# Kernel tuning notes

Measured on AMD Instinct MI355X. Metric: run time of the kernel, lower is better.

## Reference

```python
import jax, jax.numpy as jnp
import numpy as np

N = 8192
D_IN = 512
D_HID = 256
D_OUT = 128
NEG_SLOPE = 0.25
MASK_VAL = -1.0e12
EDGE_PROB = 0.004  # avg degree ~33


def _leaky(x):
    return jax.nn.leaky_relu(x, NEG_SLOPE)


def setup_inputs() -> dict:
    key = jax.random.key(0)
    ks = jax.random.split(key, 9)
    x = jax.random.normal(ks[0], (N, D_IN), jnp.float32)
    # sparse-ish normalized adjacency, stored dense (torch uses sparse mm / to_dense)
    vals = jax.random.uniform(ks[1], (N, N), jnp.float32)
    mask = jax.random.uniform(ks[2], (N, N)) < EDGE_PROB
    adj = jnp.where(mask, vals, 0.0).astype(jnp.float32)
    W1 = jax.random.normal(ks[3], (D_IN, D_HID), jnp.float32) * (2.0 / (D_IN + D_HID)) ** 0.5
    b1 = jnp.zeros((D_HID,), jnp.float32)
    W2 = jax.random.normal(ks[4], (D_HID, D_HID), jnp.float32) * (1.0 / D_HID) ** 0.5
    b2 = jnp.zeros((D_HID,), jnp.float32)
    Wg = jax.random.normal(ks[5], (D_HID, D_OUT), jnp.float32) * (2.0 / (D_HID + D_OUT)) ** 0.5
    a = jax.random.normal(ks[6], (2 * D_OUT, 1), jnp.float32) * 0.1
    return dict(x=x, adj=adj, W1=W1, b1=b1, W2=W2, b2=b2, Wg=Wg, a=a)


def reference(x, adj, W1, b1, W2, b2, Wg, a):
    # GCN layer 1: adj @ (x @ W1) + b1, leaky_relu (dropout p=0 / eval -> identity)
    x1 = _leaky(adj @ (x @ W1) + b1)
    # GCN layer 2
    x2 = _leaky(adj @ (x1 @ W2) + b2)
    # GAT layer: h = x2 @ Wg; e[i,j] = leaky_relu([h_i || h_j] @ a)
    # identical to leaky_relu((h@a1)_i + (h@a2)_j) without the O(N^2*2F) concat
    h = x2 @ Wg                              # [N, D_OUT]
    a1 = a[:D_OUT, 0]
    a2 = a[D_OUT:, 0]
    e = _leaky((h @ a1)[:, None] + (h @ a2)[None, :])  # [N, N]
    att = jnp.where(adj > 0, e, MASK_VAL)
    att = jax.nn.softmax(att, axis=1)
    h_prime = att @ h                        # [N, D_OUT] (concat=False -> no elu)
    out = _leaky(h_prime)
    mu = out[:, : D_OUT // 2]
    logvar = out[:, D_OUT // 2 :]
    return mu, logvar
```

## Files before the change

kernel.cpp:

```cpp
#include <hip/hip_runtime.h>

typedef unsigned short u16;
typedef u16 u16x4 __attribute__((ext_vector_type(4)));
typedef __bf16 bf16x8 __attribute__((ext_vector_type(8)));
typedef float f32x4 __attribute__((ext_vector_type(4)));

#define NROW 8192
#define CAP 128
#define D_IN 512
#define D_HID 256
#define D_OUT 128

__device__ __forceinline__ float leaky_f(float x) { return x > 0.f ? x : 0.25f * x; }

__device__ __forceinline__ u16 f2bf_rne(float f) {
  unsigned u = __float_as_uint(f);
  u += 0x7fffu + ((u >> 16) & 1u);
  return (u16)(u >> 16);
}
__device__ __forceinline__ float bf2f(u16 v) { return __uint_as_float(((unsigned)v) << 16); }
__device__ __forceinline__ void split_bf16(float f, u16& hi, u16& lo) {
  hi = f2bf_rne(f);
  float fh = __uint_as_float(((unsigned)hi) << 16);
  lo = f2bf_rne(f - fh);
}

__global__ __launch_bounds__(256) void k_packw(
    const float* __restrict__ W1, u16* __restrict__ B1,
    const float* __restrict__ W2, u16* __restrict__ B2,
    const float* __restrict__ Wg, u16* __restrict__ B3) {
  const float* W; u16* Bt; int K, Nc, id;
  int pb = blockIdx.x;
  if (pb < 512)      { W = W1; Bt = B1; K = D_IN;  Nc = D_HID; id = pb * 256 + threadIdx.x; }
  else if (pb < 768) { W = W2; Bt = B2; K = D_HID; Nc = D_HID; id = (pb - 512) * 256 + threadIdx.x; }
  else               { W = Wg; Bt = B3; K = D_HID; Nc = D_OUT; id = (pb - 768) * 256 + threadIdx.x; }
  int n = id % Nc, k = id / Nc;
  float f = W[id];
  u16 hi, lo; split_bf16(f, hi, lo);
  size_t ro = (size_t)n * 2 * K;
  Bt[ro + k] = hi; Bt[ro + K + k] = lo;
}

__global__ __launch_bounds__(256) void k_csr_gemm1(const float* __restrict__ adj,
    int* __restrict__ cnt, int* __restrict__ cols, float* __restrict__ vals,
    const float* __restrict__ X, const u16* __restrict__ Bt, float* __restrict__ C) {
  __shared__ u16 Ah[64 * 40], Al[64 * 40];
  __shared__ u16 Bh[64 * 40], Bl[64 * 40];
  __shared__ int csrc;
  int b = blockIdx.x;
  int tid = threadIdx.x;
  if (b < 512) {
    const int N = D_HID, K = D_IN;
    int bm = (b >> 2) * 64, bn = (b & 3) * 64;
    int wave = tid >> 6, lane = tid & 63, l15 = lane & 15, quad = lane >> 4;
    f32x4 acc[4] = {};
    int ar = tid >> 2, aj = (tid & 3) << 3;
    const float* Xrow = X + (size_t)(bm + ar) * K + aj;
    const u16* Brow = Bt + (size_t)(bn + ar) * (2 * K) + aj;
    for (int k0 = 0; k0 < K; k0 += 32) {
      alignas(16) u16 hh[8], ll[8];
      float xv[8];
      *(float4*)(xv)     = *(const float4*)(Xrow + k0);
      *(float4*)(xv + 4) = *(const float4*)(Xrow + k0 + 4);
#pragma unroll
      for (int e = 0; e < 8; ++e) split_bf16(xv[e], hh[e], ll[e]);
      *(uint4*)(&Ah[ar * 40 + aj]) = *(const uint4*)hh;
      *(uint4*)(&Al[ar * 40 + aj]) = *(const uint4*)ll;
      *(uint4*)(&Bh[ar * 40 + aj]) = *(const uint4*)(Brow + k0);
      *(uint4*)(&Bl[ar * 40 + aj]) = *(const uint4*)(Brow + K + k0);
      __syncthreads();
      bf16x8 afh = *(const bf16x8*)(&Ah[(wave * 16 + l15) * 40 + quad * 8]);
      bf16x8 afl = *(const bf16x8*)(&Al[(wave * 16 + l15) * 40 + quad * 8]);
#pragma unroll
      for (int c = 0; c < 4; ++c) {
        bf16x8 bfh = *(const bf16x8*)(&Bh[(c * 16 + l15) * 40 + quad * 8]);
        bf16x8 bfl = *(const bf16x8*)(&Bl[(c * 16 + l15) * 40 + quad * 8]);
        acc[c] = __builtin_amdgcn_mfma_f32_16x16x32_bf16(afh, bfh, acc[c], 0, 0, 0);
        acc[c] = __builtin_amdgcn_mfma_f32_16x16x32_bf16(afh, bfl, acc[c], 0, 0, 0);
        acc[c] = __builtin_amdgcn_mfma_f32_16x16x32_bf16(afl, bfh, acc[c], 0, 0, 0);
      }
      __syncthreads();
    }
#pragma unroll
    for (int c = 0; c < 4; ++c)
#pragma unroll
      for (int rg = 0; rg < 4; ++rg) {
        int rowi = bm + wave * 16 + quad * 4 + rg;
        int coli = bn + c * 16 + l15;
        C[(size_t)rowi * N + coli] = acc[c][rg];
      }
    return;
  }
  int i = b - 512;
  if (tid == 0) csrc = 0;
  __syncthreads();
  const float4* row = (const float4*)(adj + (size_t)i * NROW);
  for (int j4 = tid; j4 < NROW / 4; j4 += 256) {
    float4 v = row[j4];
    int base = j4 * 4;
    if (v.x > 0.f) { int s = atomicAdd(&csrc, 1); if (s < CAP) { cols[i*CAP+s] = base;   vals[i*CAP+s] = v.x; } }
    if (v.y > 0.f) { int s = atomicAdd(&csrc, 1); if (s < CAP) { cols[i*CAP+s] = base+1; vals[i*CAP+s] = v.y; } }
    if (v.z > 0.f) { int s = atomicAdd(&csrc, 1); if (s < CAP) { cols[i*CAP+s] = base+2; vals[i*CAP+s] = v.z; } }
    if (v.w > 0.f) { int s = atomicAdd(&csrc, 1); if (s < CAP) { cols[i*CAP+s] = base+3; vals[i*CAP+s] = v.w; } }
  }
  __syncthreads();
  if (tid == 0) cnt[i] = (csrc < CAP) ? csrc : CAP;
}

__global__ __launch_bounds__(256) void k_gemm(const u16* __restrict__ A, const u16* __restrict__ Bt,
    float* __restrict__ C, int N, int K) {
  __shared__ u16 Ah[64 * 40], Al[64 * 40];
  __shared__ u16 Bh[64 * 40], Bl[64 * 40];
  int tid = threadIdx.x;
  int bm = blockIdx.y * 64, bn = blockIdx.x * 64;
  int wave = tid >> 6, lane = tid & 63, l15 = lane & 15, quad = lane >> 4;
  f32x4 acc[4] = {};
  int ar = tid >> 2, aj = (tid & 3) << 3;
  const u16* Arow = A + (size_t)(bm + ar) * (2 * K) + aj;
  const u16* Brow = Bt + (size_t)(bn + ar) * (2 * K) + aj;
  for (int k0 = 0; k0 < K; k0 += 32) {
    *(uint4*)(&Ah[ar * 40 + aj]) = *(const uint4*)(Arow + k0);
    *(uint4*)(&Al[ar * 40 + aj]) = *(const uint4*)(Arow + K + k0);
    *(uint4*)(&Bh[ar * 40 + aj]) = *(const uint4*)(Brow + k0);
    *(uint4*)(&Bl[ar * 40 + aj]) = *(const uint4*)(Brow + K + k0);
    __syncthreads();
    bf16x8 afh = *(const bf16x8*)(&Ah[(wave * 16 + l15) * 40 + quad * 8]);
    bf16x8 afl = *(const bf16x8*)(&Al[(wave * 16 + l15) * 40 + quad * 8]);
#pragma unroll
    for (int c = 0; c < 4; ++c) {
      bf16x8 bfh = *(const bf16x8*)(&Bh[(c * 16 + l15) * 40 + quad * 8]);
      bf16x8 bfl = *(const bf16x8*)(&Bl[(c * 16 + l15) * 40 + quad * 8]);
      acc[c] = __builtin_amdgcn_mfma_f32_16x16x32_bf16(afh, bfh, acc[c], 0, 0, 0);
      acc[c] = __builtin_amdgcn_mfma_f32_16x16x32_bf16(afh, bfl, acc[c], 0, 0, 0);
      acc[c] = __builtin_amdgcn_mfma_f32_16x16x32_bf16(afl, bfh, acc[c], 0, 0, 0);
    }
    __syncthreads();
  }
#pragma unroll
  for (int c = 0; c < 4; ++c)
#pragma unroll
    for (int rg = 0; rg < 4; ++rg) {
      int rowi = bm + wave * 16 + quad * 4 + rg;
      int coli = bn + c * 16 + l15;
      C[(size_t)rowi * N + coli] = acc[c][rg];
    }
}

__global__ __launch_bounds__(256) void k_gemm3(const u16* __restrict__ A, const u16* __restrict__ Bt,
    u16* __restrict__ Hb, int K,
    const float* __restrict__ aptr, float* __restrict__ s1, float* __restrict__ s2) {
  __shared__ u16 Ah[32 * 40], Al[32 * 40];
  __shared__ u16 Bh[128 * 40], Bl[128 * 40];
  __shared__ float sp1[2][32], sp2[2][32];
  int tid = threadIdx.x;
  int bm = blockIdx.y * 32;
  int wave = tid >> 6, lane = tid & 63, l15 = lane & 15, quad = lane >> 4;
  int rhalf = wave >> 1, chalf = wave & 1;
  f32x4 acc[4] = {};
  int t7 = tid & 127;
  int ar = t7 >> 2, aj = (t7 & 3) << 3;
  int br = tid >> 1, bj = (tid & 1) << 4;
  const u16* Arow = A + (size_t)(bm + ar) * (2 * K) + aj + (tid < 128 ? 0 : K);
  u16* Adst = (tid < 128 ? Ah : Al) + ar * 40 + aj;
  const u16* Brow = Bt + (size_t)br * (2 * K) + bj;
  for (int k0 = 0; k0 < K; k0 += 32) {
    *(uint4*)Adst = *(const uint4*)(Arow + k0);
#pragma unroll
    for (int jj = 0; jj < 2; ++jj) {
      *(uint4*)(&Bh[br * 40 + bj + jj * 8]) = *(const uint4*)(Brow + k0 + jj * 8);
      *(uint4*)(&Bl[br * 40 + bj + jj * 8]) = *(const uint4*)(Brow + K + k0 + jj * 8);
    }
    __syncthreads();
    bf16x8 afh = *(const bf16x8*)(&Ah[(rhalf * 16 + l15) * 40 + quad * 8]);
    bf16x8 afl = *(const bf16x8*)(&Al[(rhalf * 16 + l15) * 40 + quad * 8]);
#pragma unroll
    for (int c = 0; c < 4; ++c) {
      bf16x8 bfh = *(const bf16x8*)(&Bh[(chalf * 64 + c * 16 + l15) * 40 + quad * 8]);
      bf16x8 bfl = *(const bf16x8*)(&Bl[(chalf * 64 + c * 16 + l15) * 40 + quad * 8]);
      acc[c] = __builtin_amdgcn_mfma_f32_16x16x32_bf16(afh, bfh, acc[c], 0, 0, 0);
      acc[c] = __builtin_amdgcn_mfma_f32_16x16x32_bf16(afh, bfl, acc[c], 0, 0, 0);
      acc[c] = __builtin_amdgcn_mfma_f32_16x16x32_bf16(afl, bfh, acc[c], 0, 0, 0);
    }
    __syncthreads();
  }
#pragma unroll
  for (int c = 0; c < 4; ++c)
#pragma unroll
    for (int rg = 0; rg < 4; ++rg) {
      int rowi = bm + rhalf * 16 + quad * 4 + rg;
      int coli = chalf * 64 + c * 16 + l15;
      Hb[(size_t)rowi * 128 + coli] = f2bf_rne(acc[c][rg]);
    }
  float a1v[4], a2v[4];
#pragma unroll
  for (int c = 0; c < 4; ++c) {
    a1v[c] = aptr[chalf * 64 + c * 16 + l15];
    a2v[c] = aptr[128 + chalf * 64 + c * 16 + l15];
  }
#pragma unroll
  for (int rg = 0; rg < 4; ++rg) {
    float p1 = 0.f, p2 = 0.f;
#pragma unroll
    for (int c = 0; c < 4; ++c) { p1 = fmaf(acc[c][rg], a1v[c], p1); p2 = fmaf(acc[c][rg], a2v[c], p2); }
#pragma unroll
    for (int m = 1; m < 16; m <<= 1) { p1 += __shfl_xor(p1, m); p2 += __shfl_xor(p2, m); }
    if (l15 == 0) {
      int rloc = rhalf * 16 + quad * 4 + rg;
      sp1[chalf][rloc] = p1; sp2[chalf][rloc] = p2;
    }
  }
  __syncthreads();
  if (tid < 32) {
    s1[bm + tid] = sp1[0][tid] + sp1[1][tid];
    s2[bm + tid] = sp2[0][tid] + sp2[1][tid];
  }
}

__global__ __launch_bounds__(256) void k_spmm_pack(const float* __restrict__ Hin,
    const float* __restrict__ bias, const int* __restrict__ cnt,
    const int* __restrict__ cols, const float* __restrict__ vals, u16* __restrict__ Ap) {
  int i = blockIdx.x, t = threadIdx.x;
  int t64 = t & 63, g = t >> 6;
  __shared__ int sc[CAP];
  __shared__ float sv[CAP];
  __shared__ float4 sacc[4][64];
  int n = cnt[i];
  if (t < n) { sc[t] = cols[i * CAP + t]; sv[t] = vals[i * CAP + t]; }
  __syncthreads();
  float4 acc = {0.f, 0.f, 0.f, 0.f};
  const float4* H4 = (const float4*)Hin;
  for (int k = g; k < n; k += 4) {
    float w = sv[k];
    float4 v = H4[(size_t)sc[k] * 64 + t64];
    acc.x = fmaf(w, v.x, acc.x); acc.y = fmaf(w, v.y, acc.y);
    acc.z = fmaf(w, v.z, acc.z); acc.w = fmaf(w, v.w, acc.w);
  }
  sacc[g][t64] = acc;
  __syncthreads();
  if (t < 64) {
    float4 a0 = sacc[0][t], a1 = sacc[1][t], a2 = sacc[2][t], a3 = sacc[3][t];
    float4 bv = ((const float4*)bias)[t];
    float r[4] = { leaky_f(a0.x + a1.x + a2.x + a3.x + bv.x),
                   leaky_f(a0.y + a1.y + a2.y + a3.y + bv.y),
                   leaky_f(a0.z + a1.z + a2.z + a3.z + bv.z),
                   leaky_f(a0.w + a1.w + a2.w + a3.w + bv.w) };
    u16x4 hi4, lo4;
#pragma unroll
    for (int e = 0; e < 4; ++e) { u16 hh, ll; split_bf16(r[e], hh, ll); hi4[e] = hh; lo4[e] = ll; }
    size_t ro = (size_t)i * 512;
    *(u16x4*)(Ap + ro + 4 * t) = hi4;
    *(u16x4*)(Ap + ro + 256 + 4 * t) = lo4;
  }
}

__global__ __launch_bounds__(128) void k_attn(const u16* __restrict__ Hb,
    const float* __restrict__ s1, const float* __restrict__ s2,
    const int* __restrict__ cnt, const int* __restrict__ cols, float* __restrict__ out) {
  int i = blockIdx.x, t = threadIdx.x;
  int t32 = t & 31, g = t >> 5;
  __shared__ int sc[CAP];
  __shared__ float sw[CAP];
  __shared__ float sred[2];
  __shared__ float4 sacc[4][32];
  int n = cnt[i];
  float s1i = s1[i];
  if (t < n) { int c = cols[i * CAP + t]; sc[t] = c; sw[t] = leaky_f(s1i + s2[c]); }
  __syncthreads();
  if (t < 64) {
    float m = -1e30f;
    if (t < n) m = sw[t];
    if (t + 64 < n) m = fmaxf(m, sw[t + 64]);
    for (int o = 32; o > 0; o >>= 1) m = fmaxf(m, __shfl_down(m, o));
    if (t == 0) sred[0] = m;
  }
  __syncthreads();
  float mx = sred[0];
  if (t < n) sw[t] = expf(sw[t] - mx);
  __syncthreads();
  if (t < 64) {
    float s = 0.f;
    if (t < n) s = sw[t];
    if (t + 64 < n) s += sw[t + 64];
    for (int o = 32; o > 0; o >>= 1) s += __shfl_down(s, o);
    if (t == 0) sred[1] = s;
  }
  __syncthreads();
  float inv = (n > 0) ? 1.0f / sred[1] : 0.f;
  float4 acc = {0.f, 0.f, 0.f, 0.f};
  for (int k = g; k < n; k += 4) {
    float w = sw[k];
    u16x4 v = *(const u16x4*)(Hb + (size_t)sc[k] * 128 + 4 * t32);
    acc.x = fmaf(w, bf2f(v[0]), acc.x); acc.y = fmaf(w, bf2f(v[1]), acc.y);
    acc.z = fmaf(w, bf2f(v[2]), acc.z); acc.w = fmaf(w, bf2f(v[3]), acc.w);
  }
  sacc[g][t32] = acc;
  __syncthreads();
  if (t < 32) {
    float4 a0 = sacc[0][t], a1 = sacc[1][t], a2 = sacc[2][t], a3 = sacc[3][t];
    float4 r;
    r.x = leaky_f((a0.x + a1.x + a2.x + a3.x) * inv);
    r.y = leaky_f((a0.y + a1.y + a2.y + a3.y) * inv);
    r.z = leaky_f((a0.z + a1.z + a2.z + a3.z) * inv);
    r.w = leaky_f((a0.w + a1.w + a2.w + a3.w) * inv);
    float4* o4 = (float4*)out;
    if (t < 16) o4[(size_t)i * 16 + t] = r;
    else        o4[(size_t)NROW * 16 + (size_t)i * 16 + (t - 16)] = r;
  }
}

extern "C" void kernel_launch(void* const* d_in, const int* in_sizes, int n_in,
                              void* d_out, int out_size, void* d_ws, size_t ws_size,
                              hipStream_t stream) {
  const float* x   = (const float*)d_in[0];
  const float* adj = (const float*)d_in[1];
  const float* W1  = (const float*)d_in[2];
  const float* b1  = (const float*)d_in[3];
  const float* W2  = (const float*)d_in[4];
  const float* b2  = (const float*)d_in[5];
  const float* Wg  = (const float*)d_in[6];
  const float* a   = (const float*)d_in[7];
  float* out = (float*)d_out;

  char* ws = (char*)d_ws;
  int*   row_cnt  = (int*)  (ws + 0);
  int*   row_cols = (int*)  (ws + 32768);
  float* row_vals = (float*)(ws + 4227072);
  u16*   B1t      = (u16*)  (ws + 8421376);
  u16*   B2t      = (u16*)  (ws + 8945664);
  u16*   B3t      = (u16*)  (ws + 9207808);
  float* s1       = (float*)(ws + 9338880);
  float* s2       = (float*)(ws + 9371648);
  u16*   hbf      = (u16*)  (ws + 9404416);
  float* H0T2     = (float*)(ws + 13598720);
  u16*   Apack    = (u16*)  (ws + 21987328);

  k_packw<<<896, 256, 0, stream>>>(W1, B1t, W2, B2t, Wg, B3t);
  k_csr_gemm1<<<512 + NROW, 256, 0, stream>>>(adj, row_cnt, row_cols, row_vals, x, B1t, H0T2);
  k_spmm_pack<<<NROW, 256, 0, stream>>>(H0T2, b1, row_cnt, row_cols, row_vals, Apack);
  k_gemm<<<dim3(4, 128), 256, 0, stream>>>(Apack, B2t, H0T2, D_HID, D_HID);
  k_spmm_pack<<<NROW, 256, 0, stream>>>(H0T2, b2, row_cnt, row_cols, row_vals, Apack);
  k_gemm3<<<dim3(1, 256), 256, 0, stream>>>(Apack, B3t, hbf, D_HID, a, s1, s2);
  k_attn<<<NROW, 128, 0, stream>>>(hbf, s1, s2, row_cnt, row_cols, out);
}
```

Baseline: 471.9 us.

## Fuse sparse aggregation with following dense GEMM in layers two and three

Each sparse adjacency aggregation (bias, leaky ReLU, bf16 hi/lo split) now runs inside the same kernel as the following dense GEMM. Sixteen aggregated rows are kept in shared memory and fed directly to MFMA, which removes the packed activation round-trip through global memory and two kernel launches. In exchange only 512 blocks are launched, and each wave gathers its rows serially without the previous 4-way split over neighbours. Every block also reloads the full weight matrix, so occupancy and gather latency may suffer.

```diff
diff --git a/kernel.cpp b/kernel.cpp
--- a/kernel.cpp
+++ b/kernel.cpp
@@ -107,32 +107,60 @@
   if (tid == 0) cnt[i] = (csrc < CAP) ? csrc : CAP;
 }
 
-__global__ __launch_bounds__(256) void k_gemm(const u16* __restrict__ A, const u16* __restrict__ Bt,
-    float* __restrict__ C, int N, int K) {
-  __shared__ u16 Ah[64 * 40], Al[64 * 40];
-  __shared__ u16 Bh[64 * 40], Bl[64 * 40];
-  int tid = threadIdx.x;
-  int bm = blockIdx.y * 64, bn = blockIdx.x * 64;
-  int wave = tid >> 6, lane = tid & 63, l15 = lane & 15, quad = lane >> 4;
-  f32x4 acc[4] = {};
-  int ar = tid >> 2, aj = (tid & 3) << 3;
-  const u16* Arow = A + (size_t)(bm + ar) * (2 * K) + aj;
-  const u16* Brow = Bt + (size_t)(bn + ar) * (2 * K) + aj;
-  for (int k0 = 0; k0 < K; k0 += 32) {
-    *(uint4*)(&Ah[ar * 40 + aj]) = *(const uint4*)(Arow + k0);
-    *(uint4*)(&Al[ar * 40 + aj]) = *(const uint4*)(Arow + K + k0);
-    *(uint4*)(&Bh[ar * 40 + aj]) = *(const uint4*)(Brow + k0);
-    *(uint4*)(&Bl[ar * 40 + aj]) = *(const uint4*)(Brow + K + k0);
-    __syncthreads();
-    bf16x8 afh = *(const bf16x8*)(&Ah[(wave * 16 + l15) * 40 + quad * 8]);
-    bf16x8 afl = *(const bf16x8*)(&Al[(wave * 16 + l15) * 40 + quad * 8]);
+__global__ __launch_bounds__(256) void k_spmm_gemm2(const float* __restrict__ Hin,
+    const float* __restrict__ bias, const int* __restrict__ cnt,
+    const int* __restrict__ cols, const float* __restrict__ vals,
+    const u16* __restrict__ Bt, float* __restrict__ T2) {
+  __shared__ u16 Ahh[16 * 264], All[16 * 264];
+  __shared__ u16 Bh[256 * 40], Bl[256 * 40];
+  __shared__ int scw[4][CAP];
+  __shared__ float svw[4][CAP];
+  int tid = threadIdx.x, wave = tid >> 6, lane = tid & 63;
+  int base = blockIdx.x * 16;
+  const float4* H4 = (const float4*)Hin;
+  float4 bv = ((const float4*)bias)[lane];
+  for (int rr = 0; rr < 4; ++rr) {
+    int row = base + wave * 4 + rr;
+    int n = cnt[row];
+    if (lane < n)      { scw[wave][lane]      = cols[row*CAP+lane];      svw[wave][lane]      = vals[row*CAP+lane]; }
+    if (lane + 64 < n) { scw[wave][lane+64]   = cols[row*CAP+lane+64];   svw[wave][lane+64]   = vals[row*CAP+lane+64]; }
+    __syncthreads();
+    float4 acc = {0.f, 0.f, 0.f, 0.f};
+    for (int k = 0; k < n; ++k) {
+      float w = svw[wave][k];
+      float4 v = H4[(size_t)scw[wave][k] * 64 + lane];
+      acc.x = fmaf(w, v.x, acc.x); acc.y = fmaf(w, v.y, acc.y);
+      acc.z = fmaf(w, v.z, acc.z); acc.w = fmaf(w, v.w, acc.w);
+    }
+    float r[4] = { leaky_f(acc.x + bv.x), leaky_f(acc.y + bv.y),
+                   leaky_f(acc.z + bv.z), leaky_f(acc.w + bv.w) };
+    u16x4 hi4, lo4;
+#pragma unroll
+    for (int e = 0; e < 4; ++e) { u16 hh, ll; split_bf16(r[e], hh, ll); hi4[e] = hh; lo4[e] = ll; }
+    int ra = wave * 4 + rr;
+    *(u16x4*)(&Ahh[ra * 264 + lane * 4]) = hi4;
+    *(u16x4*)(&All[ra * 264 + lane * 4]) = lo4;
+    __syncthreads();
+  }
+  int l15 = lane & 15, quad = lane >> 4;
+  f32x4 acc2[4] = {};
+  for (int k0 = 0; k0 < 256; k0 += 32) {
+    const u16* Brow = Bt + (size_t)tid * 512 + k0;
+#pragma unroll
+    for (int j = 0; j < 4; ++j) {
+      *(uint4*)(&Bh[tid * 40 + j * 8]) = *(const uint4*)(Brow + j * 8);
+      *(uint4*)(&Bl[tid * 40 + j * 8]) = *(const uint4*)(Brow + 256 + j * 8);
+    }
+    __syncthreads();
+    bf16x8 afh = *(const bf16x8*)(&Ahh[l15 * 264 + k0 + quad * 8]);
+    bf16x8 afl = *(const bf16x8*)(&All[l15 * 264 + k0 + quad * 8]);
 #pragma unroll
     for (int c = 0; c < 4; ++c) {
-      bf16x8 bfh = *(const bf16x8*)(&Bh[(c * 16 + l15) * 40 + quad * 8]);
-      bf16x8 bfl = *(const bf16x8*)(&Bl[(c * 16 + l15) * 40 + quad * 8]);
-      acc[c] = __builtin_amdgcn_mfma_f32_16x16x32_bf16(afh, bfh, acc[c], 0, 0, 0);
-      acc[c] = __builtin_amdgcn_mfma_f32_16x16x32_bf16(afh, bfl, acc[c], 0, 0, 0);
-      acc[c] = __builtin_amdgcn_mfma_f32_16x16x32_bf16(afl, bfh, acc[c], 0, 0, 0);
+      bf16x8 bfh = *(const bf16x8*)(&Bh[(wave * 64 + c * 16 + l15) * 40 + quad * 8]);
+      bf16x8 bfl = *(const bf16x8*)(&Bl[(wave * 64 + c * 16 + l15) * 40 + quad * 8]);
+      acc2[c] = __builtin_amdgcn_mfma_f32_16x16x32_bf16(afh, bfh, acc2[c], 0, 0, 0);
+      acc2[c] = __builtin_amdgcn_mfma_f32_16x16x32_bf16(afh, bfl, acc2[c], 0, 0, 0);
+      acc2[c] = __builtin_amdgcn_mfma_f32_16x16x32_bf16(afl, bfh, acc2[c], 0, 0, 0);
     }
     __syncthreads();
   }
@@ -140,116 +168,97 @@
   for (int c = 0; c < 4; ++c)
 #pragma unroll
     for (int rg = 0; rg < 4; ++rg) {
-      int rowi = bm + wave * 16 + quad * 4 + rg;
-      int coli = bn + c * 16 + l15;
-      C[(size_t)rowi * N + coli] = acc[c][rg];
-    }
-}
-
-__global__ __launch_bounds__(256) void k_gemm3(const u16* __restrict__ A, const u16* __restrict__ Bt,
-    u16* __restrict__ Hb, int K,
+      int rowi = base + quad * 4 + rg;
+      int coli = wave * 64 + c * 16 + l15;
+      T2[(size_t)rowi * 256 + coli] = acc2[c][rg];
+    }
+}
+
+__global__ __launch_bounds__(256) void k_spmm_gemm3(const float* __restrict__ Hin,
+    const float* __restrict__ bias, const int* __restrict__ cnt,
+    const int* __restrict__ cols, const float* __restrict__ vals,
+    const u16* __restrict__ Bt, u16* __restrict__ Hb,
     const float* __restrict__ aptr, float* __restrict__ s1, float* __restrict__ s2) {
-  __shared__ u16 Ah[32 * 40], Al[32 * 40];
+  __shared__ u16 Ahh[16 * 264], All[16 * 264];
   __shared__ u16 Bh[128 * 40], Bl[128 * 40];
-  __shared__ float sp1[2][32], sp2[2][32];
-  int tid = threadIdx.x;
-  int bm = blockIdx.y * 32;
-  int wave = tid >> 6, lane = tid & 63, l15 = lane & 15, quad = lane >> 4;
-  int rhalf = wave >> 1, chalf = wave & 1;
-  f32x4 acc[4] = {};
-  int t7 = tid & 127;
-  int ar = t7 >> 2, aj = (t7 & 3) << 3;
-  int br = tid >> 1, bj = (tid & 1) << 4;
-  const u16* Arow = A + (size_t)(bm + ar) * (2 * K) + aj + (tid < 128 ? 0 : K);
-  u16* Adst = (tid < 128 ? Ah : Al) + ar * 40 + aj;
-  const u16* Brow = Bt + (size_t)br * (2 * K) + bj;
-  for (int k0 = 0; k0 < K; k0 += 32) {
-    *(uint4*)Adst = *(const uint4*)(Arow + k0);
-#pragma unroll
-    for (int jj = 0; jj < 2; ++jj) {
-      *(uint4*)(&Bh[br * 40 + bj + jj * 8]) = *(const uint4*)(Brow + k0 + jj * 8);
-      *(uint4*)(&Bl[br * 40 + bj + jj * 8]) = *(const uint4*)(Brow + K + k0 + jj * 8);
-    }
-    __syncthreads();
-    bf16x8 afh = *(const bf16x8*)(&Ah[(rhalf * 16 + l15) * 40 + quad * 8]);
-    bf16x8 afl = *(const bf16x8*)(&Al[(rhalf * 16 + l15) * 40 + quad * 8]);
-#pragma unroll
-    for (int c = 0; c < 4; ++c) {
-      bf16x8 bfh = *(const bf16x8*)(&Bh[(chalf * 64 + c * 16 + l15) * 40 + quad * 8]);
-      bf16x8 bfl = *(const bf16x8*)(&Bl[(chalf * 64 + c * 16 + l15) * 40 + quad * 8]);
-      acc[c] = __builtin_amdgcn_mfma_f32_16x16x32_bf16(afh, bfh, acc[c], 0, 0, 0);
-      acc[c] = __builtin_amdgcn_mfma_f32_16x16x32_bf16(afh, bfl, acc[c], 0, 0, 0);
-      acc[c] = __builtin_amdgcn_mfma_f32_16x16x32_bf16(afl, bfh, acc[c], 0, 0, 0);
-    }
-    __syncthreads();
-  }
-#pragma unroll
-  for (int c = 0; c < 4; ++c)
+  __shared__ int scw[4][CAP];
+  __shared__ float svw[4][CAP];
+  __shared__ float sp1[4][16], sp2[4][16];
+  int tid = threadIdx.x, wave = tid >> 6, lane = tid & 63;
+  int base = blockIdx.x * 16;
+  const float4* H4 = (const float4*)Hin;
+  float4 bv = ((const float4*)bias)[lane];
+  for (int rr = 0; rr < 4; ++rr) {
+    int row = base + wave * 4 + rr;
+    int n = cnt[row];
+    if (lane < n)      { scw[wave][lane]      = cols[row*CAP+lane];      svw[wave][lane]      = vals[row*CAP+lane]; }
+    if (lane + 64 < n) { scw[wave][lane+64]   = cols[row*CAP+lane+64];   svw[wave][lane+64]   = vals[row*CAP+lane+64]; }
+    __syncthreads();
+    float4 acc = {0.f, 0.f, 0.f, 0.f};
+    for (int k = 0; k < n; ++k) {
+      float w = svw[wave][k];
+      float4 v = H4[(size_t)scw[wave][k] * 64 + lane];
+      acc.x = fmaf(w, v.x, acc.x); acc.y = fmaf(w, v.y, acc.y);
+      acc.z = fmaf(w, v.z, acc.z); acc.w = fmaf(w, v.w, acc.w);
+    }
+    float r[4] = { leaky_f(acc.x + bv.x), leaky_f(acc.y + bv.y),
+                   leaky_f(acc.z + bv.z), leaky_f(acc.w + bv.w) };
+    u16x4 hi4, lo4;
+#pragma unroll
+    for (int e = 0; e < 4; ++e) { u16 hh, ll; split_bf16(r[e], hh, ll); hi4[e] = hh; lo4[e] = ll; }
+    int ra = wave * 4 + rr;
+    *(u16x4*)(&Ahh[ra * 264 + lane * 4]) = hi4;
+    *(u16x4*)(&All[ra * 264 + lane * 4]) = lo4;
+    __syncthreads();
+  }
+  int l15 = lane & 15, quad = lane >> 4;
+  f32x4 acc2[2] = {};
+  for (int k0 = 0; k0 < 256; k0 += 32) {
+    int n = tid & 127, half = tid >> 7;
+    const u16* Brow = Bt + (size_t)n * 512 + half * 256 + k0;
+    u16* dst = (half ? Bl : Bh) + n * 40;
+#pragma unroll
+    for (int j = 0; j < 4; ++j)
+      *(uint4*)(dst + j * 8) = *(const uint4*)(Brow + j * 8);
+    __syncthreads();
+    bf16x8 afh = *(const bf16x8*)(&Ahh[l15 * 264 + k0 + quad * 8]);
+    bf16x8 afl = *(const bf16x8*)(&All[l15 * 264 + k0 + quad * 8]);
+#pragma unroll
+    for (int c = 0; c < 2; ++c) {
+      bf16x8 bfh = *(const bf16x8*)(&Bh[((wave * 2 + c) * 16 + l15) * 40 + quad * 8]);
+      bf16x8 bfl = *(const bf16x8*)(&Bl[((wave * 2 + c) * 16 + l15) * 40 + quad * 8]);
+      acc2[c] = __builtin_amdgcn_mfma_f32_16x16x32_bf16(afh, bfh, acc2[c], 0, 0, 0);
+      acc2[c] = __builtin_amdgcn_mfma_f32_16x16x32_bf16(afh, bfl, acc2[c], 0, 0, 0);
+      acc2[c] = __builtin_amdgcn_mfma_f32_16x16x32_bf16(afl, bfh, acc2[c], 0, 0, 0);
+    }
+    __syncthreads();
+  }
+#pragma unroll
+  for (int c = 0; c < 2; ++c)
 #pragma unroll
     for (int rg = 0; rg < 4; ++rg) {
-      int rowi = bm + rhalf * 16 + quad * 4 + rg;
-      int coli = chalf * 64 + c * 16 + l15;
-      Hb[(size_t)rowi * 128 + coli] = f2bf_rne(acc[c][rg]);
-    }
-  float a1v[4], a2v[4];
-#pragma unroll
-  for (int c = 0; c < 4; ++c) {
-    a1v[c] = aptr[chalf * 64 + c * 16 + l15];
-    a2v[c] = aptr[128 + chalf * 64 + c * 16 + l15];
+      int rowi = base + quad * 4 + rg;
+      int coli = wave * 32 + c * 16 + l15;
+      Hb[(size_t)rowi * 128 + coli] = f2bf_rne(acc2[c][rg]);
+    }
+  float a1v[2], a2v[2];
+#pragma unroll
+  for (int c = 0; c < 2; ++c) {
+    a1v[c] = aptr[wave * 32 + c * 16 + l15];
+    a2v[c] = aptr[128 + wave * 32 + c * 16 + l15];
   }
 #pragma unroll
   for (int rg = 0; rg < 4; ++rg) {
-    float p1 = 0.f, p2 = 0.f;
-#pragma unroll
-    for (int c = 0; c < 4; ++c) { p1 = fmaf(acc[c][rg], a1v[c], p1); p2 = fmaf(acc[c][rg], a2v[c], p2); }
+    float p1 = fmaf(acc2[0][rg], a1v[0], acc2[1][rg] * a1v[1]);
+    float p2 = fmaf(acc2[0][rg], a2v[0], acc2[1][rg] * a2v[1]);
 #pragma unroll
     for (int m = 1; m < 16; m <<= 1) { p1 += __shfl_xor(p1, m); p2 += __shfl_xor(p2, m); }
-    if (l15 == 0) {
-      int rloc = rhalf * 16 + quad * 4 + rg;
-      sp1[chalf][rloc] = p1; sp2[chalf][rloc] = p2;
-    }
-  }
-  __syncthreads();
-  if (tid < 32) {
-    s1[bm + tid] = sp1[0][tid] + sp1[1][tid];
-    s2[bm + tid] = sp2[0][tid] + sp2[1][tid];
-  }
-}
-
-__global__ __launch_bounds__(256) void k_spmm_pack(const float* __restrict__ Hin,
-    const float* __restrict__ bias, const int* __restrict__ cnt,
-    const int* __restrict__ cols, const float* __restrict__ vals, u16* __restrict__ Ap) {
-  int i = blockIdx.x, t = threadIdx.x;
-  int t64 = t & 63, g = t >> 6;
-  __shared__ int sc[CAP];
-  __shared__ float sv[CAP];
-  __shared__ float4 sacc[4][64];
-  int n = cnt[i];
-  if (t < n) { sc[t] = cols[i * CAP + t]; sv[t] = vals[i * CAP + t]; }
-  __syncthreads();
-  float4 acc = {0.f, 0.f, 0.f, 0.f};
-  const float4* H4 = (const float4*)Hin;
-  for (int k = g; k < n; k += 4) {
-    float w = sv[k];
-    float4 v = H4[(size_t)sc[k] * 64 + t64];
-    acc.x = fmaf(w, v.x, acc.x); acc.y = fmaf(w, v.y, acc.y);
-    acc.z = fmaf(w, v.z, acc.z); acc.w = fmaf(w, v.w, acc.w);
-  }
-  sacc[g][t64] = acc;
-  __syncthreads();
-  if (t < 64) {
-    float4 a0 = sacc[0][t], a1 = sacc[1][t], a2 = sacc[2][t], a3 = sacc[3][t];
-    float4 bv = ((const float4*)bias)[t];
-    float r[4] = { leaky_f(a0.x + a1.x + a2.x + a3.x + bv.x),
-                   leaky_f(a0.y + a1.y + a2.y + a3.y + bv.y),
-                   leaky_f(a0.z + a1.z + a2.z + a3.z + bv.z),
-                   leaky_f(a0.w + a1.w + a2.w + a3.w + bv.w) };
-    u16x4 hi4, lo4;
-#pragma unroll
-    for (int e = 0; e < 4; ++e) { u16 hh, ll; split_bf16(r[e], hh, ll); hi4[e] = hh; lo4[e] = ll; }
-    size_t ro = (size_t)i * 512;
-    *(u16x4*)(Ap + ro + 4 * t) = hi4;
-    *(u16x4*)(Ap + ro + 256 + 4 * t) = lo4;
+    if (l15 == 0) { sp1[wave][quad * 4 + rg] = p1; sp2[wave][quad * 4 + rg] = p2; }
+  }
+  __syncthreads();
+  if (tid < 16) {
+    s1[base + tid] = sp1[0][tid] + sp1[1][tid] + sp1[2][tid] + sp1[3][tid];
+    s2[base + tid] = sp2[0][tid] + sp2[1][tid] + sp2[2][tid] + sp2[3][tid];
   }
 }
 
@@ -331,14 +340,12 @@
   float* s1       = (float*)(ws + 9338880);
   float* s2       = (float*)(ws + 9371648);
   u16*   hbf      = (u16*)  (ws + 9404416);
-  float* H0T2     = (float*)(ws + 13598720);
-  u16*   Apack    = (u16*)  (ws + 21987328);
+  float* H0       = (float*)(ws + 13598720);
+  float* T2       = (float*)(ws + 21987328);
 
   k_packw<<<896, 256, 0, stream>>>(W1, B1t, W2, B2t, Wg, B3t);
-  k_csr_gemm1<<<512 + NROW, 256, 0, stream>>>(adj, row_cnt, row_cols, row_vals, x, B1t, H0T2);
-  k_spmm_pack<<<NROW, 256, 0, stream>>>(H0T2, b1, row_cnt, row_cols, row_vals, Apack);
-  k_gemm<<<dim3(4, 128), 256, 0, stream>>>(Apack, B2t, H0T2, D_HID, D_HID);
-  k_spmm_pack<<<NROW, 256, 0, stream>>>(H0T2, b2, row_cnt, row_cols, row_vals, Apack);
-  k_gemm3<<<dim3(1, 256), 256, 0, stream>>>(Apack, B3t, hbf, D_HID, a, s1, s2);
+  k_csr_gemm1<<<512 + NROW, 256, 0, stream>>>(adj, row_cnt, row_cols, row_vals, x, B1t, H0);
+  k_spmm_gemm2<<<512, 256, 0, stream>>>(H0, b1, row_cnt, row_cols, row_vals, B2t, T2);
+  k_spmm_gemm3<<<512, 256, 0, stream>>>(T2, b2, row_cnt, row_cols, row_vals, B3t, hbf, a, s1, s2);
   k_attn<<<NROW, 128, 0, stream>>>(hbf, s1, s2, row_cnt, row_cols, out);
 }
```

Result: no change. 478.6 us (+1.4%).
